# Optimization experiments

Measured on AMD Instinct MI355X. Metric: run time of the kernel, lower is better.

Reference implementation:

```python
import jax, jax.numpy as jnp
import numpy as np
from jax import lax

HEADS, DIM_HEAD = 4, 64
INNER = HEADS * DIM_HEAD              # 256
FEAT_DIM = MAP_DIM = OUT_DIM = 128
EXPANDED = 4 * OUT_DIM                # 512 (MBConv expansion)
MAP_SIZE = (8, 8, 8)
EPS = 1e-5


def conv3d(x, w, groups=1):
    # x: NCDHW, w: OIDHW ([out, in/groups, kd, kh, kw]); stride 1, 'same' padding
    return lax.conv_general_dilated(x, w, (1, 1, 1), 'SAME',
                                    feature_group_count=groups,
                                    dimension_numbers=('NCDHW', 'OIDHW', 'NCDHW'))


def inorm(x):
    # InstanceNorm3d (affine=False): normalize over spatial dims per sample/channel
    m = x.mean((2, 3, 4), keepdims=True)
    v = ((x - m) ** 2).mean((2, 3, 4), keepdims=True)
    return (x - m) * lax.rsqrt(v + EPS)


def _split_heads(t, spatial):
    # 'b (dim_head heads) d h w -> b heads (d h w) dim_head'
    B = t.shape[0]
    N = spatial[0] * spatial[1] * spatial[2]
    return t.reshape(B, DIM_HEAD, HEADS, N).transpose(0, 2, 3, 1)


def _merge_heads(t, spatial):
    # 'b heads n dim_head -> b (dim_head heads) d h w'
    B = t.shape[0]
    return t.transpose(0, 3, 1, 2).reshape(B, DIM_HEAD * HEADS, *spatial)


def setup_inputs() -> dict:
    key = jax.random.key(0)
    ks = jax.random.split(key, 16)
    r = lambda k, s: jax.random.normal(k, s, jnp.float32) * 0.05
    return {
        'x': jax.random.normal(ks[0], (2, FEAT_DIM, 24, 24, 24), jnp.float32),
        'semantic_map': jax.random.normal(ks[1], (2, MAP_DIM) + MAP_SIZE, jnp.float32),
        'w_fqv_dw': r(ks[2], (FEAT_DIM, 1, 3, 3, 3)),
        'w_fqv_pw': r(ks[3], (2 * INNER, FEAT_DIM, 1, 1, 1)),
        'w_mqv':    r(ks[4], (2 * INNER, MAP_DIM, 1, 1, 1)),
        'w_fout_dw': r(ks[5], (INNER, 1, 3, 3, 3)),
        'w_fout_pw': r(ks[6], (OUT_DIM, INNER, 1, 1, 1)),
        'w_mout':   r(ks[7], (MAP_DIM, INNER, 1, 1, 1)),
        'w_exp':    r(ks[8], (EXPANDED, OUT_DIM, 1, 1, 1)),
        'w_dw':     r(ks[9], (EXPANDED, 1, 3, 3, 3)),
        'w_se1':    r(ks[10], (EXPANDED // 4, EXPANDED, 1, 1, 1)),
        'b_se1':    jnp.zeros((EXPANDED // 4,), jnp.float32),
        'w_se2':    r(ks[11], (EXPANDED, EXPANDED // 4, 1, 1, 1)),
        'b_se2':    jnp.zeros((EXPANDED,), jnp.float32),
        'w_pw':     r(ks[12], (OUT_DIM, EXPANDED, 1, 1, 1)),
    }


def _mbconv(x, w_exp, w_dw, w_se1, b_se1, w_se2, b_se2, w_pw):
    # MBConv (preact ConvNormAct blocks, InstanceNorm + ReLU, SE, identity shortcut)
    h = conv3d(jax.nn.relu(inorm(x)), w_exp)
    h = conv3d(jax.nn.relu(inorm(h)), w_dw, groups=EXPANDED)
    s = h.mean((2, 3, 4), keepdims=True)                       # squeeze
    s = jax.nn.relu(conv3d(s, w_se1) + b_se1[None, :, None, None, None])
    s = jax.nn.sigmoid(conv3d(s, w_se2) + b_se2[None, :, None, None, None])
    h = h * s
    h = conv3d(inorm(h), w_pw)                                 # pointwise, act=False
    return h + x


def reference(x, semantic_map, w_fqv_dw, w_fqv_pw, w_mqv, w_fout_dw, w_fout_pw,
              w_mout, w_exp, w_dw, w_se1, b_se1, w_se2, b_se2, w_pw):
    B, C, D, H, W = x.shape
    feat = inorm(x)
    m = inorm(semantic_map)

    # QV projections: depthwise-separable for feat, 1x1 for map
    fqv = conv3d(conv3d(feat, w_fqv_dw, groups=FEAT_DIM), w_fqv_pw)
    fq, fv = jnp.split(fqv, 2, axis=1)
    mqv = conv3d(m, w_mqv)
    mq, mv = jnp.split(mqv, 2, axis=1)

    fq = _split_heads(fq, (D, H, W))   # [B, h, Nf, dh]
    fv = _split_heads(fv, (D, H, W))
    mq = _split_heads(mq, MAP_SIZE)    # [B, h, Nm, dh]
    mv = _split_heads(mv, MAP_SIZE)

    # shared score matrix, dual-direction softmax
    attn = jnp.einsum('bhid,bhjd->bhij', fq, mq) * (DIM_HEAD ** -0.5)
    feat_map_attn = jax.nn.softmax(attn, axis=-1)   # over map tokens j
    map_feat_attn = jax.nn.softmax(attn, axis=-2)   # over feat tokens i

    feat_out = jnp.einsum('bhij,bhjd->bhid', feat_map_attn, mv)   # [B,h,Nf,dh]
    map_out = jnp.einsum('bhji,bhjd->bhid', map_feat_attn, fv)    # [B,h,Nm,dh]

    feat_out = _merge_heads(feat_out, (D, H, W))
    map_out = _merge_heads(map_out, MAP_SIZE)

    feat_out = conv3d(conv3d(feat_out, w_fout_dw, groups=INNER), w_fout_pw)
    map_out = conv3d(map_out, w_mout)

    out = feat_out + x   # shortcut is identity (feat_dim == out_dim)
    out = _mbconv(out, w_exp, w_dw, w_se1, b_se1, w_se2, b_se2, w_pw)
    map_out = map_out + semantic_map
    return out, map_out
```

## Files before the change

### kernel.cpp

```cpp
#include <hip/hip_runtime.h>
#include <hip/hip_bf16.h>
#include <cstddef>

#define NF 13824
#define NM 512
#define NIC 27

typedef __attribute__((ext_vector_type(8))) short bf16x8;
typedef __attribute__((ext_vector_type(4))) float f32x4;

__device__ __forceinline__ void gload16(const float* g, float* l){
  __builtin_amdgcn_global_load_lds((const __attribute__((address_space(1))) void*)g,
                                   (__attribute__((address_space(3))) void*)l, 16, 0, 0);
}

__global__ void k_transpose6(const float* __restrict__ s0, float* __restrict__ d0,
                             const float* __restrict__ s1, float* __restrict__ d1,
                             const float* __restrict__ s2, float* __restrict__ d2,
                             const float* __restrict__ s3, float* __restrict__ d3,
                             const float* __restrict__ s4, float* __restrict__ d4,
                             const float* __restrict__ s5, float* __restrict__ d5){
  const float* W; float* WT; int Cout, Cin;
  switch (blockIdx.y){
    case 0: W=s0; WT=d0; Cout=512; Cin=128; break;
// ... 113 lines not shown

  {
    float4* l4 = (float4*)lds;
    float4 z = make_float4(0.f,0.f,0.f,0.f);
    for (int i=threadIdx.x; i<(4+26*728)/4; i+=256) l4[i] = z;
  }
  __syncthreads();

  const float* pin = in + (size_t)bc*NF;
  for (int i=threadIdx.x; i<NF/4; i+=256){
    int n = i*4;
    int d = n/576, r2 = n%576;
    int h = r2/24, wq = r2%24;
    float4 v = *(const float4*)(pin + n);
    float v0 = a*v.x+bb, v1 = a*v.y+bb, v2 = a*v.z+bb, v3 = a*v.w+bb;
    if (relu){ v0=fmaxf(v0,0.f); v1=fmaxf(v1,0.f); v2=fmaxf(v2,0.f); v3=fmaxf(v3,0.f); }
    *(float4*)(lds + 4 + (d+1)*728 + (h+1)*28 + wq) = make_float4(v0,v1,v2,v3);
  }

  const float* wc = w + c*27;
  float wr[27];
  #pragma unroll
  for (int k=0;k<27;k++) wr[k] = wc[k];
  __syncthreads();

  float ss=0.f, sq=0.f;
  for (int r = threadIdx.x; r < 576; r += 256){
    int d = r/24, h = r%24;
    float acc[24];
    #pragma unroll
    for (int i=0;i<24;i++) acc[i] = 0.f;
    #pragma unroll
    for (int kd=0;kd<3;kd++){
      #pragma unroll
      for (int kh=0;kh<3;kh++){
        const float* row = lds + 4 + (d+kd)*728 + (h+kh)*28;
        float rr[24];
        #pragma unroll
        for (int q=0;q<6;q++){
          float4 v4 = *(const float4*)(row + 4*q);
          rr[4*q]=v4.x; rr[4*q+1]=v4.y; rr[4*q+2]=v4.z; rr[4*q+3]=v4.w;
        }
        float rl = row[-1];
        float rrgt = row[24];
        float w0 = wr[kd*9+kh*3+0], w1 = wr[kd*9+kh*3+1], w2 = wr[kd*9+kh*3+2];
        acc[0] += w0*rl + w1*rr[0] + w2*rr[1];
        #pragma unroll
        for (int i=1;i<23;i++) acc[i] += w0*rr[i-1] + w1*rr[i] + w2*rr[i+1];
        acc[23] += w0*rr[22] + w1*rr[23] + w2*rrgt;
      }
    }
    if (stout){
      #pragma unroll
      for (int i=0;i<24;i++){ ss += acc[i]; sq += acc[i]*acc[i]; }
    }
    float* op = out + (size_t)bc*NF + r*24;
    #pragma unroll
    for (int q=0;q<6;q++)
      *(float4*)(op + 4*q) = make_float4(acc[4*q],acc[4*q+1],acc[4*q+2],acc[4*q+3]);
  }
  if (stout){
    rs2[threadIdx.x]=ss; rq2[threadIdx.x]=sq;
    __syncthreads();
    for (int o=128;o>0;o>>=1){
      if (threadIdx.x<o){ rs2[threadIdx.x]+=rs2[threadIdx.x+o]; rq2[threadIdx.x]+=rq2[threadIdx.x+o]; }
      __syncthreads();
    }
    if (threadIdx.x==0){
      float m = rs2[0]/NF;
      float v = rq2[0]/NF - m*m;
      stout[bc] = make_float2(m, v>0.f? v:0.f);
    }
  }
}

__global__ __launch_bounds__(256) void k_pw2(const float* __restrict__ in, const float* __restrict__ Wt,
                    const float* __restrict__ bias,
                    int Cin, int Cout, int N, int wstride,
                    const float* __restrict__ res,
                    float* __restrict__ out0,
                    __hip_bfloat16* __restrict__ qnm, __hip_bfloat16* __restrict__ vdm,
                    int mode, float2* __restrict__ part, int nparts){
  int b = blockIdx.z;
  int n0 = blockIdx.x*64, co0 = blockIdx.y*64;
  int tx = threadIdx.x & 15, ty = threadIdx.x >> 4;
  int wv = threadIdx.x >> 6, ln = threadIdx.x & 63;
  __shared__ float wl[2][2048];
  __shared__ float il[2][2048];
  float acc[4][4] = {};
  const float* inb = in + (size_t)b*Cin*N;
  const float* wb  = Wt + (size_t)b*wstride;

  int row0 = wv*8 + (ln>>4), col = (ln&15)*4;
  int row1 = row0 + 4;
  const float* gw0 = wb  + (size_t)row0*Cout + co0 + col;
  const float* gw1 = wb  + (size_t)row1*Cout + co0 + col;
  const float* gi0 = inb + (size_t)row0*N + n0 + col;
  const float* gi1 = inb + (size_t)row1*N + n0 + col;
  int lb0 = wv*512, lb1 = wv*512 + 256;

  gload16(gw0, &wl[0][lb0]); gload16(gw1, &wl[0][lb1]);
  gload16(gi0, &il[0][lb0]); gload16(gi1, &il[0][lb1]);
  __syncthreads();

  int nc = Cin >> 5;
  int cur = 0;
  for (int c=0; c<nc; c++){
    if (c+1 < nc){
      size_t ow = (size_t)(c+1)*32*Cout, oi = (size_t)(c+1)*32*N;
      gload16(gw0+ow, &wl[cur^1][lb0]); gload16(gw1+ow, &wl[cur^1][lb1]);
      gload16(gi0+oi, &il[cur^1][lb0]); gload16(gi1+oi, &il[cur^1][lb1]);
    }
    #pragma unroll
    for (int ci=0;ci<32;ci++){
      float4 a4 = *(const float4*)&wl[cur][ci*64 + ty*4];
      float4 b4 = *(const float4*)&il[cur][ci*64 + tx*4];
      acc[0][0]+=a4.x*b4.x; acc[0][1]+=a4.x*b4.y; acc[0][2]+=a4.x*b4.z; acc[0][3]+=a4.x*b4.w;
      acc[1][0]+=a4.y*b4.x; acc[1][1]+=a4.y*b4.y; acc[1][2]+=a4.y*b4.z; acc[1][3]+=a4.y*b4.w;
      acc[2][0]+=a4.z*b4.x; acc[2][1]+=a4.z*b4.y; acc[2][2]+=a4.z*b4.z; acc[2][3]+=a4.z*b4.w;
      acc[3][0]+=a4.w*b4.x; acc[3][1]+=a4.w*b4.y; acc[3][2]+=a4.w*b4.z; acc[3][3]+=a4.w*b4.w;
    }
    __syncthreads();
    cur ^= 1;
  }

  if (mode==0){
    #pragma unroll
    for (int i=0;i<4;i++){
      int co = co0 + ty*4 + i;
      float bco = bias ? bias[b*Cout + co] : 0.f;
      float* op = out0 + ((size_t)b*Cout + co)*N;
      float sv=0.f, qv=0.f;
      #pragma unroll
      for (int j=0;j<4;j++){
        int n = n0 + tx*4 + j;
        float v = acc[i][j] + bco;
        if (res) v += res[((size_t)b*Cout + co)*N + n];
        op[n] = v;
        sv += v; qv += v*v;
      }
      if (part){
        sv += __shfl_xor(sv,1); sv += __shfl_xor(sv,2); sv += __shfl_xor(sv,4); sv += __shfl_xor(sv,8);
        qv += __shfl_xor(qv,1); qv += __shfl_xor(qv,2); qv += __shfl_xor(qv,4); qv += __shfl_xor(qv,8);
        if (tx==0)
          part[(size_t)(b*Cout + co)*nparts + blockIdx.x] = make_float2(sv, qv);
      }
    }
  } else {
    int ccbase = (co0 & 255) + ty*4;
    int dd = ccbase >> 2;
    bool isq = (co0 < 256);
    #pragma unroll
    for (int i=0;i<4;i++){
      int bhid = b*4 + i;
      #pragma unroll
      for (int j=0;j<4;j++){
        int n = n0 + tx*4 + j;
        __hip_bfloat16 v = __float2bfloat16(acc[i][j]);
        if (isq) qnm[((size_t)bhid*N + n)*64 + dd] = v;
        else     vdm[((size_t)(bhid*64 + dd))*N + n] = v;
      }
    }
  }
}

__global__ __launch_bounds__(256) void k_pw(const float* __restrict__ in, const float* __restrict__ WT,
                    const float2* __restrict__ tf, int relu,
                    int Cin, int Cout, int N,
                    const float* __restrict__ res,
                    float* __restrict__ out0,
                    __hip_bfloat16* __restrict__ qnm, __hip_bfloat16* __restrict__ vdm,
                    int mode){
  int b = blockIdx.z;
  int n0 = blockIdx.x*64, co0 = blockIdx.y*64;
  int tx = threadIdx.x & 15, ty = threadIdx.x >> 4;
  int cc = threadIdx.x & 63, g = threadIdx.x >> 6;
  __shared__ float wl[32][68];
  __shared__ float il[32][68];
  float acc[4][4] = {};
  const float* inb = in + (size_t)b*Cin*N;

  float rw[8], rv[8], ta[8], tb[8];
  #pragma unroll
  for (int rr=0;rr<8;rr++){ ta[rr]=1.f; tb[rr]=0.f; }
  #pragma unroll
  for (int rr=0;rr<8;rr++){
    int ci = g + 4*rr;
    rw[rr] = WT[(size_t)ci*Cout + co0 + cc];
    rv[rr] = inb[(size_t)ci*N + n0 + cc];
    if (tf){ float2 t = tf[b*Cin + ci]; ta[rr]=t.x; tb[rr]=t.y; }
  }

  for (int c0=0;c0<Cin;c0+=32){
    __syncthreads();
    #pragma unroll
    for (int rr=0;rr<8;rr++){
      int ci = g + 4*rr;
      wl[ci][cc] = rw[rr];
      float v = ta[rr]*rv[rr] + tb[rr];
      if (relu) v = fmaxf(v, 0.f);
      il[ci][cc] = v;
    }
    __syncthreads();
    if (c0+32 < Cin){
      int c0n = c0+32;
      #pragma unroll
      for (int rr=0;rr<8;rr++){
        int ci = g + 4*rr;
        rw[rr] = WT[(size_t)(c0n+ci)*Cout + co0 + cc];
        rv[rr] = inb[(size_t)(c0n+ci)*N + n0 + cc];
        if (tf){ float2 t = tf[b*Cin + c0n + ci]; ta[rr]=t.x; tb[rr]=t.y; }
      }
    }
    #pragma unroll
    for (int ci=0;ci<32;ci++){
      float4 a4 = *(const float4*)&wl[ci][ty*4];
      float4 b4 = *(const float4*)&il[ci][tx*4];
      acc[0][0]+=a4.x*b4.x; acc[0][1]+=a4.x*b4.y; acc[0][2]+=a4.x*b4.z; acc[0][3]+=a4.x*b4.w;
      acc[1][0]+=a4.y*b4.x; acc[1][1]+=a4.y*b4.y; acc[1][2]+=a4.y*b4.z; acc[1][3]+=a4.y*b4.w;
      acc[2][0]+=a4.z*b4.x; acc[2][1]+=a4.z*b4.y; acc[2][2]+=a4.z*b4.z; acc[2][3]+=a4.z*b4.w;
      acc[3][0]+=a4.w*b4.x; acc[3][1]+=a4.w*b4.y; acc[3][2]+=a4.w*b4.z; acc[3][3]+=a4.w*b4.w;
    }
  }
  if (mode==0){
    #pragma unroll
    for (int i=0;i<4;i++){
      int co = co0 + ty*4 + i;
      float* op = out0 + ((size_t)b*Cout + co)*N;
      #pragma unroll
      for (int j=0;j<4;j++){
        int n = n0 + tx*4 + j;
        float v = acc[i][j];
        if (res) v += res[((size_t)b*Cout + co)*N + n];
        op[n] = v;
      }
    }
  } else {
    int ccbase = (co0 & 255) + ty*4;
    int dd = ccbase >> 2;
    bool isq = (co0 < 256);
    #pragma unroll
    for (int i=0;i<4;i++){
      int bhid = b*4 + i;
      #pragma unroll
      for (int j=0;j<4;j++){
        int n = n0 + tx*4 + j;
        __hip_bfloat16 v = __float2bfloat16(acc[i][j]);
        if (isq) qnm[((size_t)bhid*N + n)*64 + dd] = v;
        else     vdm[((size_t)(bhid*64 + dd))*N + n] = v;
      }
    }
  }
}

__global__ __launch_bounds__(256) void k_fattn(const __hip_bfloat16* __restrict__ qf,
    const __hip_bfloat16* __restrict__ qm, const __hip_bfloat16* __restrict__ vm,
    float* __restrict__ fo){
  int bh = blockIdx.y, b = bh>>2, h = bh&3;
  int w = threadIdx.x>>6, l = threadIdx.x&63;
  int i0 = blockIdx.x*128 + w*32;
  int lr = l&15, lg = l>>4;
  __shared__ __hip_bfloat16 pl[4][2][2][16][40];
  __shared__ float rsl[4][32];
  bf16x8 aq[2][2];
  #pragma unroll
  for (int g=0; g<2; g++){
    const __hip_bfloat16* qb = qf + ((size_t)bh*NF + i0 + g*16 + lr)*64 + lg*8;
    aq[g][0] = *(const bf16x8*)(qb);
    aq[g][1] = *(const bf16x8*)(qb + 32);
  }
  f32x4 facc[2][4];
  #pragma unroll
  for (int g=0; g<2; g++)
    #pragma unroll
    for (int t=0;t<4;t++){ facc[g][t][0]=0.f; facc[g][t][1]=0.f; facc[g][t][2]=0.f; facc[g][t][3]=0.f; }
  float rs[2][4] = {};
  const __hip_bfloat16* kbase = qm + ((size_t)bh*NM + lr)*64 + lg*8;
  const __hip_bfloat16* vbase = vm + ((size_t)bh*64 + lr)*NM + lg*8;

  auto fcomp = [&](bf16x8 K0, bf16x8 K1, bf16x8 K2, bf16x8 K3,
                   bf16x8 V0, bf16x8 V1, bf16x8 V2, bf16x8 V3, int SET){
    #pragma unroll
    for (int g=0; g<2; g++){
      f32x4 s0 = {0.f,0.f,0.f,0.f}, s1 = {0.f,0.f,0.f,0.f};
      s0 = __builtin_amdgcn_mfma_f32_16x16x32_bf16(aq[g][0], K0, s0, 0,0,0);
      s0 = __builtin_amdgcn_mfma_f32_16x16x32_bf16(aq[g][1], K1, s0, 0,0,0);
      s1 = __builtin_amdgcn_mfma_f32_16x16x32_bf16(aq[g][0], K2, s1, 0,0,0);
      s1 = __builtin_amdgcn_mfma_f32_16x16x32_bf16(aq[g][1], K3, s1, 0,0,0);
      #pragma unroll
      for (int r=0;r<4;r++){
        float p0 = __expf(s0[r]*0.125f);
        float p1 = __expf(s1[r]*0.125f);
        pl[w][SET][g][4*lg+r][lr]    = __float2bfloat16(p0);
        pl[w][SET][g][4*lg+r][16+lr] = __float2bfloat16(p1);
        rs[g][r] += p0 + p1;
      }
    }
    #pragma unroll
    for (int g=0; g<2; g++){
      bf16x8 bp = *(const bf16x8*)&pl[w][SET][g][lr][lg*8];
      facc[g][0] = __builtin_amdgcn_mfma_f32_16x16x32_bf16(V0, bp, facc[g][0], 0,0,0);
      facc[g][1] = __builtin_amdgcn_mfma_f32_16x16x32_bf16(V1, bp, facc[g][1], 0,0,0);
      facc[g][2] = __builtin_amdgcn_mfma_f32_16x16x32_bf16(V2, bp, facc[g][2], 0,0,0);
      facc[g][3] = __builtin_amdgcn_mfma_f32_16x16x32_bf16(V3, bp, facc[g][3], 0,0,0);
    }
  };

  bf16x8 kA0,kA1,kA2,kA3,vA0,vA1,vA2,vA3;
  bf16x8 kB0,kB1,kB2,kB3,vB0,vB1,vB2,vB3;
  #define FLOAD(KP,VP,J0) \
    KP##0 = *(const bf16x8*)(kbase + (size_t)(J0)*64); \
    KP##1 = *(const bf16x8*)(kbase + (size_t)(J0)*64 + 32); \
    KP##2 = *(const bf16x8*)(kbase + (size_t)(J0)*64 + 1024); \
    KP##3 = *(const bf16x8*)(kbase + (size_t)(J0)*64 + 1056); \
    VP##0 = *(const bf16x8*)(vbase + (J0)); \
    VP##1 = *(const bf16x8*)(vbase + 16*NM + (J0)); \
    VP##2 = *(const bf16x8*)(vbase + 32*NM + (J0)); \
    VP##3 = *(const bf16x8*)(vbase + 48*NM + (J0));

  FLOAD(kA,vA,0)
  for (int jt=0; jt<16; jt+=2){
    FLOAD(kB,vB,(jt+1)*32)
    fcomp(kA0,kA1,kA2,kA3,vA0,vA1,vA2,vA3,0);
    if (jt+2 < 16){ FLOAD(kA,vA,(jt+2)*32) }
    fcomp(kB0,kB1,kB2,kB3,vB0,vB1,vB2,vB3,1);
  }
  #undef FLOAD

  #pragma unroll
  for (int g=0; g<2; g++)
    #pragma unroll
    for (int r=0;r<4;r++){
      float v = rs[g][r];
      v += __shfl_xor(v,1); v += __shfl_xor(v,2); v += __shfl_xor(v,4); v += __shfl_xor(v,8);
      if (lr==0) rsl[w][g*16 + 4*lg+r] = v;
    }
  __syncthreads();
  #pragma unroll
  for (int g=0; g<2; g++){
    float inv = 1.f / rsl[w][g*16 + lr];
    #pragma unroll
    for (int dt=0; dt<4; dt++){
      #pragma unroll
      for (int r=0;r<4;r++){
        int d = dt*16 + 4*lg + r;
        fo[((size_t)(b*256 + d*4 + h))*NF + i0 + g*16 + lr] = facc[g][dt][r]*inv;
      }
    }
  }
}

__global__ __launch_bounds__(256) void k_mattn(const __hip_bfloat16* __restrict__ qm,
    const __hip_bfloat16* __restrict__ qf, const __hip_bfloat16* __restrict__ vf,
    float* __restrict__ num, float* __restrict__ cs){
  int ic = blockIdx.x, jb = blockIdx.y, bh = blockIdx.z;
  int w = threadIdx.x>>6, l = threadIdx.x&63;
  int lr = l&15, lg = l>>4;
  int jt0 = jb*128 + w*16;
  int jt1 = jt0 + 64;
  __shared__ __hip_bfloat16 pl[4][2][2][16][40];
  bf16x8 am[2][2];
  {
    const __hip_bfloat16* ab0 = qm + ((size_t)bh*NM + jt0 + lr)*64 + lg*8;
    const __hip_bfloat16* ab1 = qm + ((size_t)bh*NM + jt1 + lr)*64 + lg*8;
    am[0][0] = *(const bf16x8*)(ab0);
    am[0][1] = *(const bf16x8*)(ab0 + 32);
    am[1][0] = *(const bf16x8*)(ab1);
    am[1][1] = *(const bf16x8*)(ab1 + 32);
  }
  f32x4 macc[2][4];
  #pragma unroll
  for (int jg=0;jg<2;jg++)
    #pragma unroll
    for (int t=0;t<4;t++){ macc[jg][t][0]=0.f; macc[jg][t][1]=0.f; macc[jg][t][2]=0.f; macc[jg][t][3]=0.f; }
  float csr[2][4] = {};
  const __hip_bfloat16* fbase  = qf + ((size_t)bh*NF + lr)*64 + lg*8;
  const __hip_bfloat16* vfbase = vf + ((size_t)bh*64 + lr)*NF + lg*8;

  auto mcomp = [&](bf16x8 F0, bf16x8 F1, bf16x8 F2, bf16x8 F3,
                   bf16x8 V0, bf16x8 V1, bf16x8 V2, bf16x8 V3, int SET){
    #pragma unroll
    for (int jg=0;jg<2;jg++){
      f32x4 s0 = {0.f,0.f,0.f,0.f}, s1 = {0.f,0.f,0.f,0.f};
      s0 = __builtin_amdgcn_mfma_f32_16x16x32_bf16(am[jg][0], F0, s0, 0,0,0);
      s0 = __builtin_amdgcn_mfma_f32_16x16x32_bf16(am[jg][1], F1, s0, 0,0,0);
      s1 = __builtin_amdgcn_mfma_f32_16x16x32_bf16(am[jg][0], F2, s1, 0,0,0);
      s1 = __builtin_amdgcn_mfma_f32_16x16x32_bf16(am[jg][1], F3, s1, 0,0,0);
      #pragma unroll
      for (int r=0;r<4;r++){
        float p0 = __expf(s0[r]*0.125f);
        float p1 = __expf(s1[r]*0.125f);
        pl[w][SET][jg][4*lg+r][lr]    = __float2bfloat16(p0);
        pl[w][SET][jg][4*lg+r][16+lr] = __float2bfloat16(p1);
        csr[jg][r] += p0 + p1;
      }
    }
    #pragma unroll
    for (int jg=0;jg<2;jg++){
      bf16x8 bp = *(const bf16x8*)&pl[w][SET][jg][lr][lg*8];
      macc[jg][0] = __builtin_amdgcn_mfma_f32_16x16x32_bf16(V0, bp, macc[jg][0], 0,0,0);
      macc[jg][1] = __builtin_amdgcn_mfma_f32_16x16x32_bf16(V1, bp, macc[jg][1], 0,0,0);
      macc[jg][2] = __builtin_amdgcn_mfma_f32_16x16x32_bf16(V2, bp, macc[jg][2], 0,0,0);
      macc[jg][3] = __builtin_amdgcn_mfma_f32_16x16x32_bf16(V3, bp, macc[jg][3], 0,0,0);
    }
  };

  bf16x8 fA0,fA1,fA2,fA3,vA0,vA1,vA2,vA3;
  bf16x8 fB0,fB1,fB2,fB3,vB0,vB1,vB2,vB3;
  #define MLOAD(FP,VP,I0) \
    FP##0 = *(const bf16x8*)(fbase + (size_t)(I0)*64); \
    FP##1 = *(const bf16x8*)(fbase + (size_t)(I0)*64 + 32); \
    FP##2 = *(const bf16x8*)(fbase + (size_t)(I0)*64 + 1024); \
    FP##3 = *(const bf16x8*)(fbase + (size_t)(I0)*64 + 1056); \
    VP##0 = *(const bf16x8*)(vfbase + (size_t)(I0)); \
    VP##1 = *(const bf16x8*)(vfbase + (size_t)16*NF + (I0)); \
    VP##2 = *(const bf16x8*)(vfbase + (size_t)32*NF + (I0)); \
    VP##3 = *(const bf16x8*)(vfbase + (size_t)48*NF + (I0));

  int ibase = ic*512;
  MLOAD(fA,vA, ibase)
  for (int is=0; is<16; is+=2){
    MLOAD(fB,vB, ibase + (is+1)*32)
    mcomp(fA0,fA1,fA2,fA3,vA0,vA1,vA2,vA3,0);
    if (is+2<16){ MLOAD(fA,vA, ibase + (is+2)*32) }
    mcomp(fB0,fB1,fB2,fB3,vB0,vB1,vB2,vB3,1);
  }
  #undef MLOAD

  size_t nb = ((size_t)(ic*8 + bh)*64)*512;
  #pragma unroll
  for (int jg=0;jg<2;jg++){
    int jt = jg ? jt1 : jt0;
    #pragma unroll
    for (int dt=0;dt<4;dt++){
      #pragma unroll
      for (int r=0;r<4;r++){
        num[nb + (size_t)(dt*16 + 4*lg + r)*512 + jt + lr] = macc[jg][dt][r];
      }
    }
  }
  #pragma unroll
  for (int jg=0;jg<2;jg++){
    int jt = jg ? jt1 : jt0;
    #pragma unroll
    for (int r=0;r<4;r++){
      float v = csr[jg][r];
      v += __shfl_xor(v,1); v += __shfl_xor(v,2); v += __shfl_xor(v,4); v += __shfl_xor(v,8);
      if (lr==0) cs[(size_t)(ic*8 + bh)*512 + jt + 4*lg + r] = v;
    }
  }
}

__global__ void k_comb(const float* __restrict__ num, const float* __restrict__ cs,
                       float* __restrict__ ma){
  int idx = blockIdx.x*256 + threadIdx.x;
  if (idx >= 8*512*64) return;
  int bh = idx>>15; int rem = idx&32767; int j = rem>>6; int d = rem&63;
  float s=0.f, c=0.f;
  for (int ic=0;ic<NIC;ic++){
    s += num[((size_t)(ic*8+bh)*64 + d)*512 + j];
    c += cs[(size_t)(ic*8+bh)*512 + j];
  }
  int b = bh>>2, h = bh&3;
  ma[((size_t)(b*256 + d*4 + h))*NM + j] = s/c;
}

__global__ void k_se(const float2* __restrict__ st, const float* __restrict__ w1, const float* __restrict__ b1,
                     const float* __restrict__ w2, const float* __restrict__ b2, float* __restrict__ sout){
  int b = blockIdx.x; int t = threadIdx.x;
  __shared__ float mean[512]; __shared__ float s1[128];
  mean[t]     = st[b*512 + t].x;
  mean[t+256] = st[b*512 + t + 256].x;
  __syncthreads();
  if (t<128){
    float a = b1[t];
    for (int c=0;c<512;c++) a += w1[t*512+c]*mean[c];
    s1[t] = fmaxf(a, 0.f);
  }
  __syncthreads();
  for (int o=t;o<512;o+=256){
    float a = b2[o];
    for (int c=0;c<128;c++) a += w2[o*128+c]*s1[c];
    sout[b*512+o] = 1.f/(1.f+__expf(-a));
  }
}

extern "C" void kernel_launch(void* const* d_in, const int* in_sizes, int n_in,
                              void* d_out, int out_size, void* d_ws, size_t ws_size,
                              hipStream_t stream){
  const float* x     = (const float*)d_in[0];
  const float* smap  = (const float*)d_in[1];
  const float* wfdw  = (const float*)d_in[2];
  const float* wfpw  = (const float*)d_in[3];
  const float* wmqv  = (const float*)d_in[4];
  const float* wodw  = (const float*)d_in[5];
  const float* wopw  = (const float*)d_in[6];
  const float* wmout = (const float*)d_in[7];
  const float* wexp  = (const float*)d_in[8];
  const float* wdw   = (const float*)d_in[9];
  const float* wse1  = (const float*)d_in[10];
  const float* bse1  = (const float*)d_in[11];
  const float* wse2  = (const float*)d_in[12];
  const float* bse2  = (const float*)d_in[13];
  const float* wpw   = (const float*)d_in[14];

  float* out  = (float*)d_out;
  float* mout = out + (size_t)2*128*NF;

  float* W = (float*)d_ws;
  size_t o = 0;
  __hip_bfloat16* qf = (__hip_bfloat16*)(W + o); o += (size_t)8*NF*32;
  __hip_bfloat16* vf = (__hip_bfloat16*)(W + o); o += (size_t)8*NF*32;
  float* fdw  = W + o; o += (size_t)2*128*NF;
  float* num  = W + o; o += (size_t)NIC*8*64*512;
  __hip_bfloat16* qm = (__hip_bfloat16*)(W + o); o += 8*NM*32;
  __hip_bfloat16* vm = (__hip_bfloat16*)(W + o); o += 8*NM*32;
  float* csb  = W + o; o += (size_t)NIC*8*512;
  float* ma   = W + o; o += (size_t)2*256*NM;
  float* h2   = (float*)d_ws;
  float* fo   = W + o; o += (size_t)2*256*NF;
  float* fdw2 = W + o; o += (size_t)2*256*NF;
  float* h1 = fo;
  float* wTf  = W + o; o += 512*128;
  float* wTm  = W + o; o += 512*128;
  float* wTo  = W + o; o += 128*256;
  float* wTmo = W + o; o += 128*256;
  float* wTe  = W + o; o += 512*128;
  float* wTp  = W + o; o += 128*512;
  float* wfP  = W + o; o += (size_t)2*512*128;
  float* biasP= W + o; o += 2*128;
  float2* partO = (float2*)(W+o); o += (size_t)2*256*216;
  float2* partH1= (float2*)(W+o); o += (size_t)2*1024*216;
  float2* tfO = (float2*)(W+o); o += 512;
  float2* tfH1= (float2*)(W+o); o += 2048;
  float2* stA = (float2*)(W+o); o += 512;
  float2* tfA = (float2*)(W+o); o += 512;
  float2* stM = (float2*)(W+o); o += 512;
  float2* tfM = (float2*)(W+o); o += 512;
  float2* stH2= (float2*)(W+o); o += 2048;
  float2* tfH = (float2*)(W+o); o += 2048;
  float* sbuf = W + o; o += 1024;
  (void)ws_size; (void)in_sizes; (void)n_in; (void)out_size;

  k_transpose6<<<dim3(256,6),256,0,stream>>>(wfpw,wTf, wmqv,wTm, wopw,wTo, wmout,wTmo, wexp,wTe, wpw,wTp);

  k_stats<<<256,256,0,stream>>>(x, stA, NF, tfA);
  k_dw3t<<<256,256,0,stream>>>(x, wfdw, tfA, fdw, 128, 0, nullptr);
  k_pw2<<<dim3(216,8,2),256,0,stream>>>(fdw, wTf, nullptr, 128,512,NF,0, nullptr, nullptr, qf, vf, 1, nullptr,0);

  k_stats<<<256,256,0,stream>>>(smap, stM, NM, tfM);
  k_pw<<<dim3(8,8,2),256,0,stream>>>(smap, wTm, tfM,0, 128,512,NM, nullptr, nullptr, qm, vm, 1);

  k_fattn<<<dim3(108,8),256,0,stream>>>(qf, qm, vm, fo);
  k_mattn<<<dim3(NIC,4,8),256,0,stream>>>(qm, qf, vf, num, csb);
  k_comb<<<1024,256,0,stream>>>(num, csb, ma);

  k_dw3t<<<512,256,0,stream>>>(fo, wodw, nullptr, fdw2, 256, 0, nullptr);
  k_pw2<<<dim3(216,2,2),256,0,stream>>>(fdw2, wTo, nullptr, 256,128,NF,0, x, out, nullptr,nullptr, 0, partO,216);
  k_pw<<<dim3(8,2,2),256,0,stream>>>(ma, wTmo, nullptr,0, 256,128,NM, smap, mout, nullptr,nullptr, 0);

  k_red<<<64,256,0,stream>>>(partO, 216, 256, 1.f/NF, tfO);
  k_act<<<3456,256,0,stream>>>(out, tfO, fdw);
  k_pw2<<<dim3(216,8,2),256,0,stream>>>(fdw, wTe, nullptr, 128,512,NF,0, nullptr, h1, nullptr,nullptr, 0, partH1,216);

  k_red<<<256,256,0,stream>>>(partH1, 216, 1024, 1.f/NF, tfH1);
  k_dw3t<<<1024,256,0,stream>>>(h1, wdw, tfH1, h2, 512, 1, stH2);

  k_se<<<2,256,0,stream>>>(stH2, wse1,bse1,wse2,bse2, sbuf);
  k_make_tf<<<4,256,0,stream>>>(stH2, sbuf, tfH, 1024);
  k_fold<<<dim3(128,2),256,0,stream>>>(wTp, tfH, wfP, biasP);
  k_pw2<<<dim3(216,2,2),256,0,stream>>>(h2, wfP, biasP, 512,128,NF,512*128, out, out, nullptr,nullptr, 0, nullptr,0);
}
```

Before: 575.8 us.

## Widen pointwise GEMM tiles to 128 channels and fuse both attention kernels

The pointwise conv kernel now computes 128 output channels per block with an 8x4 per-thread accumulator tile. Each loaded activation tile is reused across twice as many channels, halving the grid and the redundant input reads. The feature-to-map and map-to-feature attention kernels are merged into one launch with interleaved block roles, which removes a launch and lets the two workloads overlap. The costs are higher register pressure and fewer blocks for the pointwise GEMMs, and the fused kernel takes on the larger register footprint of the two branches.

```diff
diff --git a/kernel.cpp b/kernel.cpp
--- a/kernel.cpp
+++ b/kernel.cpp
@@ -219,43 +219,53 @@
                     __hip_bfloat16* __restrict__ qnm, __hip_bfloat16* __restrict__ vdm,
                     int mode, float2* __restrict__ part, int nparts){
   int b = blockIdx.z;
-  int n0 = blockIdx.x*64, co0 = blockIdx.y*64;
-  int tx = threadIdx.x & 15, ty = threadIdx.x >> 4;
-  int wv = threadIdx.x >> 6, ln = threadIdx.x & 63;
-  __shared__ float wl[2][2048];
-  __shared__ float il[2][2048];
-  float acc[4][4] = {};
+  int n0 = blockIdx.x*64, co0 = blockIdx.y*128;
+  int t = threadIdx.x;
+  int tx = t & 15, tyy = t >> 4;
+  int wv = t >> 6, ln = t & 63;
+  __shared__ float wl[2][32*128];
+  __shared__ float il[2][32*64];
+  float acc[8][4] = {};
   const float* inb = in + (size_t)b*Cin*N;
   const float* wb  = Wt + (size_t)b*wstride;
 
-  int row0 = wv*8 + (ln>>4), col = (ln&15)*4;
-  int row1 = row0 + 4;
-  const float* gw0 = wb  + (size_t)row0*Cout + co0 + col;
-  const float* gw1 = wb  + (size_t)row1*Cout + co0 + col;
-  const float* gi0 = inb + (size_t)row0*N + n0 + col;
-  const float* gi1 = inb + (size_t)row1*N + n0 + col;
-  int lb0 = wv*512, lb1 = wv*512 + 256;
-
-  gload16(gw0, &wl[0][lb0]); gload16(gw1, &wl[0][lb1]);
-  gload16(gi0, &il[0][lb0]); gload16(gi1, &il[0][lb1]);
+  int wrow = (ln>>5), wcol = (ln&31)*4;
+  int irow = (ln>>4), icol = (ln&15)*4;
+
+  auto STAGE = [&](int c0, int buf){
+    #pragma unroll
+    for (int k=0;k<4;k++){
+      int row = wv*8 + 2*k + wrow;
+      gload16(wb + (size_t)(c0+row)*Cout + co0 + wcol, &wl[buf][row*128 + wcol]);
+    }
+    #pragma unroll
+    for (int k=0;k<2;k++){
+      int row = wv*8 + 4*k + irow;
+      gload16(inb + (size_t)(c0+row)*N + n0 + icol, &il[buf][row*64 + icol]);
+    }
+  };
+
+  STAGE(0, 0);
   __syncthreads();
 
   int nc = Cin >> 5;
   int cur = 0;
   for (int c=0; c<nc; c++){
-    if (c+1 < nc){
-      size_t ow = (size_t)(c+1)*32*Cout, oi = (size_t)(c+1)*32*N;
-      gload16(gw0+ow, &wl[cur^1][lb0]); gload16(gw1+ow, &wl[cur^1][lb1]);
-      gload16(gi0+oi, &il[cur^1][lb0]); gload16(gi1+oi, &il[cur^1][lb1]);
-    }
+    if (c+1 < nc) STAGE((c+1)*32, cur^1);
     #pragma unroll
     for (int ci=0;ci<32;ci++){
-      float4 a4 = *(const float4*)&wl[cur][ci*64 + ty*4];
+      const float* wr2 = &wl[cur][ci*128 + tyy*8];
+      float4 w0 = *(const float4*)(wr2);
+      float4 w1 = *(const float4*)(wr2+4);
       float4 b4 = *(const float4*)&il[cur][ci*64 + tx*4];
-      acc[0][0]+=a4.x*b4.x; acc[0][1]+=a4.x*b4.y; acc[0][2]+=a4.x*b4.z; acc[0][3]+=a4.x*b4.w;
-      acc[1][0]+=a4.y*b4.x; acc[1][1]+=a4.y*b4.y; acc[1][2]+=a4.y*b4.z; acc[1][3]+=a4.y*b4.w;
-      acc[2][0]+=a4.z*b4.x; acc[2][1]+=a4.z*b4.y; acc[2][2]+=a4.z*b4.z; acc[2][3]+=a4.z*b4.w;
-      acc[3][0]+=a4.w*b4.x; acc[3][1]+=a4.w*b4.y; acc[3][2]+=a4.w*b4.z; acc[3][3]+=a4.w*b4.w;
+      acc[0][0]+=w0.x*b4.x; acc[0][1]+=w0.x*b4.y; acc[0][2]+=w0.x*b4.z; acc[0][3]+=w0.x*b4.w;
+      acc[1][0]+=w0.y*b4.x; acc[1][1]+=w0.y*b4.y; acc[1][2]+=w0.y*b4.z; acc[1][3]+=w0.y*b4.w;
+      acc[2][0]+=w0.z*b4.x; acc[2][1]+=w0.z*b4.y; acc[2][2]+=w0.z*b4.z; acc[2][3]+=w0.z*b4.w;
+      acc[3][0]+=w0.w*b4.x; acc[3][1]+=w0.w*b4.y; acc[3][2]+=w0.w*b4.z; acc[3][3]+=w0.w*b4.w;
+      acc[4][0]+=w1.x*b4.x; acc[4][1]+=w1.x*b4.y; acc[4][2]+=w1.x*b4.z; acc[4][3]+=w1.x*b4.w;
+      acc[5][0]+=w1.y*b4.x; acc[5][1]+=w1.y*b4.y; acc[5][2]+=w1.y*b4.z; acc[5][3]+=w1.y*b4.w;
+      acc[6][0]+=w1.z*b4.x; acc[6][1]+=w1.z*b4.y; acc[6][2]+=w1.z*b4.z; acc[6][3]+=w1.z*b4.w;
+      acc[7][0]+=w1.w*b4.x; acc[7][1]+=w1.w*b4.y; acc[7][2]+=w1.w*b4.z; acc[7][3]+=w1.w*b4.w;
     }
     __syncthreads();
     cur ^= 1;
@@ -263,8 +273,8 @@
 
   if (mode==0){
     #pragma unroll
-    for (int i=0;i<4;i++){
-      int co = co0 + ty*4 + i;
+    for (int i=0;i<8;i++){
+      int co = co0 + tyy*8 + i;
       float bco = bias ? bias[b*Cout + co] : 0.f;
       float* op = out0 + ((size_t)b*Cout + co)*N;
       float sv=0.f, qv=0.f;
@@ -284,12 +294,12 @@
       }
     }
   } else {
-    int ccbase = (co0 & 255) + ty*4;
-    int dd = ccbase >> 2;
     bool isq = (co0 < 256);
     #pragma unroll
-    for (int i=0;i<4;i++){
-      int bhid = b*4 + i;
+    for (int i=0;i<8;i++){
+      int co = co0 + tyy*8 + i;
+      int head = co & 3, dd = (co & 255) >> 2;
+      int bhid = b*4 + head;
       #pragma unroll
       for (int j=0;j<4;j++){
         int n = n0 + tx*4 + j;
@@ -390,200 +400,199 @@
   }
 }
 
-__global__ __launch_bounds__(256) void k_fattn(const __hip_bfloat16* __restrict__ qf,
+__global__ __launch_bounds__(256) void k_attn(const __hip_bfloat16* __restrict__ qf,
     const __hip_bfloat16* __restrict__ qm, const __hip_bfloat16* __restrict__ vm,
-    float* __restrict__ fo){
-  int bh = blockIdx.y, b = bh>>2, h = bh&3;
-  int w = threadIdx.x>>6, l = threadIdx.x&63;
-  int i0 = blockIdx.x*128 + w*32;
-  int lr = l&15, lg = l>>4;
+    const __hip_bfloat16* __restrict__ vf,
+    float* __restrict__ fo, float* __restrict__ num, float* __restrict__ cs){
   __shared__ __hip_bfloat16 pl[4][2][2][16][40];
   __shared__ float rsl[4][32];
-  bf16x8 aq[2][2];
-  #pragma unroll
-  for (int g=0; g<2; g++){
-    const __hip_bfloat16* qb = qf + ((size_t)bh*NF + i0 + g*16 + lr)*64 + lg*8;
-    aq[g][0] = *(const bf16x8*)(qb);
-    aq[g][1] = *(const bf16x8*)(qb + 32);
-  }
-  f32x4 facc[2][4];
-  #pragma unroll
-  for (int g=0; g<2; g++)
-    #pragma unroll
-    for (int t=0;t<4;t++){ facc[g][t][0]=0.f; facc[g][t][1]=0.f; facc[g][t][2]=0.f; facc[g][t][3]=0.f; }
-  float rs[2][4] = {};
-  const __hip_bfloat16* kbase = qm + ((size_t)bh*NM + lr)*64 + lg*8;
-  const __hip_bfloat16* vbase = vm + ((size_t)bh*64 + lr)*NM + lg*8;
-
-  auto fcomp = [&](bf16x8 K0, bf16x8 K1, bf16x8 K2, bf16x8 K3,
-                   bf16x8 V0, bf16x8 V1, bf16x8 V2, bf16x8 V3, int SET){
-    #pragma unroll
-    for (int g=0; g<2; g++){
-      f32x4 s0 = {0.f,0.f,0.f,0.f}, s1 = {0.f,0.f,0.f,0.f};
-      s0 = __builtin_amdgcn_mfma_f32_16x16x32_bf16(aq[g][0], K0, s0, 0,0,0);
-      s0 = __builtin_amdgcn_mfma_f32_16x16x32_bf16(aq[g][1], K1, s0, 0,0,0);
-      s1 = __builtin_amdgcn_mfma_f32_16x16x32_bf16(aq[g][0], K2, s1, 0,0,0);
-      s1 = __builtin_amdgcn_mfma_f32_16x16x32_bf16(aq[g][1], K3, s1, 0,0,0);
-      #pragma unroll
-      for (int r=0;r<4;r++){
-        float p0 = __expf(s0[r]*0.125f);
-        float p1 = __expf(s1[r]*0.125f);
-        pl[w][SET][g][4*lg+r][lr]    = __float2bfloat16(p0);
-        pl[w][SET][g][4*lg+r][16+lr] = __float2bfloat16(p1);
-        rs[g][r] += p0 + p1;
-      }
-    }
-    #pragma unroll
-    for (int g=0; g<2; g++){
-      bf16x8 bp = *(const bf16x8*)&pl[w][SET][g][lr][lg*8];
-      facc[g][0] = __builtin_amdgcn_mfma_f32_16x16x32_bf16(V0, bp, facc[g][0], 0,0,0);
-      facc[g][1] = __builtin_amdgcn_mfma_f32_16x16x32_bf16(V1, bp, facc[g][1], 0,0,0);
-      facc[g][2] = __builtin_amdgcn_mfma_f32_16x16x32_bf16(V2, bp, facc[g][2], 0,0,0);
-      facc[g][3] = __builtin_amdgcn_mfma_f32_16x16x32_bf16(V3, bp, facc[g][3], 0,0,0);
-    }
-  };
-
-  bf16x8 kA0,kA1,kA2,kA3,vA0,vA1,vA2,vA3;
-  bf16x8 kB0,kB1,kB2,kB3,vB0,vB1,vB2,vB3;
-  #define FLOAD(KP,VP,J0) \
-    KP##0 = *(const bf16x8*)(kbase + (size_t)(J0)*64); \
-    KP##1 = *(const bf16x8*)(kbase + (size_t)(J0)*64 + 32); \
-    KP##2 = *(const bf16x8*)(kbase + (size_t)(J0)*64 + 1024); \
-    KP##3 = *(const bf16x8*)(kbase + (size_t)(J0)*64 + 1056); \
-    VP##0 = *(const bf16x8*)(vbase + (J0)); \
-    VP##1 = *(const bf16x8*)(vbase + 16*NM + (J0)); \
-    VP##2 = *(const bf16x8*)(vbase + 32*NM + (J0)); \
-    VP##3 = *(const bf16x8*)(vbase + 48*NM + (J0));
-
-  FLOAD(kA,vA,0)
-  for (int jt=0; jt<16; jt+=2){
-    FLOAD(kB,vB,(jt+1)*32)
-    fcomp(kA0,kA1,kA2,kA3,vA0,vA1,vA2,vA3,0);
-    if (jt+2 < 16){ FLOAD(kA,vA,(jt+2)*32) }
-    fcomp(kB0,kB1,kB2,kB3,vB0,vB1,vB2,vB3,1);
-  }
-  #undef FLOAD
-
-  #pragma unroll
-  for (int g=0; g<2; g++)
-    #pragma unroll
-    for (int r=0;r<4;r++){
-      float v = rs[g][r];
-      v += __shfl_xor(v,1); v += __shfl_xor(v,2); v += __shfl_xor(v,4); v += __shfl_xor(v,8);
-      if (lr==0) rsl[w][g*16 + 4*lg+r] = v;
-    }
-  __syncthreads();
-  #pragma unroll
-  for (int g=0; g<2; g++){
-    float inv = 1.f / rsl[w][g*16 + lr];
-    #pragma unroll
-    for (int dt=0; dt<4; dt++){
-      #pragma unroll
-      for (int r=0;r<4;r++){
-        int d = dt*16 + 4*lg + r;
-        fo[((size_t)(b*256 + d*4 + h))*NF + i0 + g*16 + lr] = facc[g][dt][r]*inv;
-      }
-    }
-  }
-}
-
-__global__ __launch_bounds__(256) void k_mattn(const __hip_bfloat16* __restrict__ qm,
-    const __hip_bfloat16* __restrict__ qf, const __hip_bfloat16* __restrict__ vf,
-    float* __restrict__ num, float* __restrict__ cs){
-  int ic = blockIdx.x, jb = blockIdx.y, bh = blockIdx.z;
+  int bid = blockIdx.x;
+  int sub = bid >> 1;
   int w = threadIdx.x>>6, l = threadIdx.x&63;
   int lr = l&15, lg = l>>4;
-  int jt0 = jb*128 + w*16;
-  int jt1 = jt0 + 64;
-  __shared__ __hip_bfloat16 pl[4][2][2][16][40];
-  bf16x8 am[2][2];
-  {
-    const __hip_bfloat16* ab0 = qm + ((size_t)bh*NM + jt0 + lr)*64 + lg*8;
-    const __hip_bfloat16* ab1 = qm + ((size_t)bh*NM + jt1 + lr)*64 + lg*8;
-    am[0][0] = *(const bf16x8*)(ab0);
-    am[0][1] = *(const bf16x8*)(ab0 + 32);
-    am[1][0] = *(const bf16x8*)(ab1);
-    am[1][1] = *(const bf16x8*)(ab1 + 32);
-  }
-  f32x4 macc[2][4];
-  #pragma unroll
-  for (int jg=0;jg<2;jg++)
-    #pragma unroll
-    for (int t=0;t<4;t++){ macc[jg][t][0]=0.f; macc[jg][t][1]=0.f; macc[jg][t][2]=0.f; macc[jg][t][3]=0.f; }
-  float csr[2][4] = {};
-  const __hip_bfloat16* fbase  = qf + ((size_t)bh*NF + lr)*64 + lg*8;
-  const __hip_bfloat16* vfbase = vf + ((size_t)bh*64 + lr)*NF + lg*8;
-
-  auto mcomp = [&](bf16x8 F0, bf16x8 F1, bf16x8 F2, bf16x8 F3,
-                   bf16x8 V0, bf16x8 V1, bf16x8 V2, bf16x8 V3, int SET){
+
+  if (bid & 1){
+    int bh = sub/108, b = bh>>2, h = bh&3;
+    int i0 = (sub%108)*128 + w*32;
+    bf16x8 aq[2][2];
+    #pragma unroll
+    for (int g=0; g<2; g++){
+      const __hip_bfloat16* qb = qf + ((size_t)bh*NF + i0 + g*16 + lr)*64 + lg*8;
+      aq[g][0] = *(const bf16x8*)(qb);
+      aq[g][1] = *(const bf16x8*)(qb + 32);
+    }
+    f32x4 facc[2][4];
+    #pragma unroll
+    for (int g=0; g<2; g++)
+      #pragma unroll
+      for (int t=0;t<4;t++){ facc[g][t][0]=0.f; facc[g][t][1]=0.f; facc[g][t][2]=0.f; facc[g][t][3]=0.f; }
+    float rs[2][4] = {};
+    const __hip_bfloat16* kbase = qm + ((size_t)bh*NM + lr)*64 + lg*8;
+    const __hip_bfloat16* vbase = vm + ((size_t)bh*64 + lr)*NM + lg*8;
+
+    auto fcomp = [&](bf16x8 K0, bf16x8 K1, bf16x8 K2, bf16x8 K3,
+                     bf16x8 V0, bf16x8 V1, bf16x8 V2, bf16x8 V3, int SET){
+      #pragma unroll
+      for (int g=0; g<2; g++){
+        f32x4 s0 = {0.f,0.f,0.f,0.f}, s1 = {0.f,0.f,0.f,0.f};
+        s0 = __builtin_amdgcn_mfma_f32_16x16x32_bf16(aq[g][0], K0, s0, 0,0,0);
+        s0 = __builtin_amdgcn_mfma_f32_16x16x32_bf16(aq[g][1], K1, s0, 0,0,0);
+        s1 = __builtin_amdgcn_mfma_f32_16x16x32_bf16(aq[g][0], K2, s1, 0,0,0);
+        s1 = __builtin_amdgcn_mfma_f32_16x16x32_bf16(aq[g][1], K3, s1, 0,0,0);
+        #pragma unroll
+        for (int r=0;r<4;r++){
+          float p0 = __expf(s0[r]*0.125f);
+          float p1 = __expf(s1[r]*0.125f);
+          pl[w][SET][g][4*lg+r][lr]    = __float2bfloat16(p0);
+          pl[w][SET][g][4*lg+r][16+lr] = __float2bfloat16(p1);
+          rs[g][r] += p0 + p1;
+        }
+      }
+      #pragma unroll
+      for (int g=0; g<2; g++){
+        bf16x8 bp = *(const bf16x8*)&pl[w][SET][g][lr][lg*8];
+        facc[g][0] = __builtin_amdgcn_mfma_f32_16x16x32_bf16(V0, bp, facc[g][0], 0,0,0);
+        facc[g][1] = __builtin_amdgcn_mfma_f32_16x16x32_bf16(V1, bp, facc[g][1], 0,0,0);
+        facc[g][2] = __builtin_amdgcn_mfma_f32_16x16x32_bf16(V2, bp, facc[g][2], 0,0,0);
+        facc[g][3] = __builtin_amdgcn_mfma_f32_16x16x32_bf16(V3, bp, facc[g][3], 0,0,0);
+      }
+    };
+
+    bf16x8 kA0,kA1,kA2,kA3,vA0,vA1,vA2,vA3;
+    bf16x8 kB0,kB1,kB2,kB3,vB0,vB1,vB2,vB3;
+    #define FLOAD(KP,VP,J0) \
+      KP##0 = *(const bf16x8*)(kbase + (size_t)(J0)*64); \
+      KP##1 = *(const bf16x8*)(kbase + (size_t)(J0)*64 + 32); \
+      KP##2 = *(const bf16x8*)(kbase + (size_t)(J0)*64 + 1024); \
+      KP##3 = *(const bf16x8*)(kbase + (size_t)(J0)*64 + 1056); \
+      VP##0 = *(const bf16x8*)(vbase + (J0)); \
+      VP##1 = *(const bf16x8*)(vbase + 16*NM + (J0)); \
+      VP##2 = *(const bf16x8*)(vbase + 32*NM + (J0)); \
+      VP##3 = *(const bf16x8*)(vbase + 48*NM + (J0));
+
+    FLOAD(kA,vA,0)
+    for (int jt=0; jt<16; jt+=2){
+      FLOAD(kB,vB,(jt+1)*32)
+      fcomp(kA0,kA1,kA2,kA3,vA0,vA1,vA2,vA3,0);
+      if (jt+2 < 16){ FLOAD(kA,vA,(jt+2)*32) }
+      fcomp(kB0,kB1,kB2,kB3,vB0,vB1,vB2,vB3,1);
+    }
+    #undef FLOAD
+
+    #pragma unroll
+    for (int g=0; g<2; g++)
+      #pragma unroll
+      for (int r=0;r<4;r++){
+        float v = rs[g][r];
+        v += __shfl_xor(v,1); v += __shfl_xor(v,2); v += __shfl_xor(v,4); v += __shfl_xor(v,8);
+        if (lr==0) rsl[w][g*16 + 4*lg+r] = v;
+      }
+    __syncthreads();
+    #pragma unroll
+    for (int g=0; g<2; g++){
+      float inv = 1.f / rsl[w][g*16 + lr];
+      #pragma unroll
+      for (int dt=0; dt<4; dt++){
+        #pragma unroll
+        for (int r=0;r<4;r++){
+          int d = dt*16 + 4*lg + r;
+          fo[((size_t)(b*256 + d*4 + h))*NF + i0 + g*16 + lr] = facc[g][dt][r]*inv;
+        }
+      }
+    }
+  } else {
+    int ic = sub%27, jb = (sub/27)&3, bh = sub/108;
+    int jt0 = jb*128 + w*16;
+    int jt1 = jt0 + 64;
+    bf16x8 am[2][2];
+    {
+      const __hip_bfloat16* ab0 = qm + ((size_t)bh*NM + jt0 + lr)*64 + lg*8;
+      const __hip_bfloat16* ab1 = qm + ((size_t)bh*NM + jt1 + lr)*64 + lg*8;
+      am[0][0] = *(const bf16x8*)(ab0);
+      am[0][1] = *(const bf16x8*)(ab0 + 32);
+      am[1][0] = *(const bf16x8*)(ab1);
+      am[1][1] = *(const bf16x8*)(ab1 + 32);
+    }
+    f32x4 macc[2][4];
+    #pragma unroll
+    for (int jg=0;jg<2;jg++)
+      #pragma unroll
+      for (int t=0;t<4;t++){ macc[jg][t][0]=0.f; macc[jg][t][1]=0.f; macc[jg][t][2]=0.f; macc[jg][t][3]=0.f; }
+    float csr[2][4] = {};
+    const __hip_bfloat16* fbase  = qf + ((size_t)bh*NF + lr)*64 + lg*8;
+    const __hip_bfloat16* vfbase = vf + ((size_t)bh*64 + lr)*NF + lg*8;
+
+    auto mcomp = [&](bf16x8 F0, bf16x8 F1, bf16x8 F2, bf16x8 F3,
+                     bf16x8 V0, bf16x8 V1, bf16x8 V2, bf16x8 V3, int SET){
+      #pragma unroll
+      for (int jg=0;jg<2;jg++){
+        f32x4 s0 = {0.f,0.f,0.f,0.f}, s1 = {0.f,0.f,0.f,0.f};
+        s0 = __builtin_amdgcn_mfma_f32_16x16x32_bf16(am[jg][0], F0, s0, 0,0,0);
+        s0 = __builtin_amdgcn_mfma_f32_16x16x32_bf16(am[jg][1], F1, s0, 0,0,0);
+        s1 = __builtin_amdgcn_mfma_f32_16x16x32_bf16(am[jg][0], F2, s1, 0,0,0);
+        s1 = __builtin_amdgcn_mfma_f32_16x16x32_bf16(am[jg][1], F3, s1, 0,0,0);
+        #pragma unroll
+        for (int r=0;r<4;r++){
+          float p0 = __expf(s0[r]*0.125f);
+          float p1 = __expf(s1[r]*0.125f);
+          pl[w][SET][jg][4*lg+r][lr]    = __float2bfloat16(p0);
+          pl[w][SET][jg][4*lg+r][16+lr] = __float2bfloat16(p1);
+          csr[jg][r] += p0 + p1;
+        }
+      }
+      #pragma unroll
+      for (int jg=0;jg<2;jg++){
+        bf16x8 bp = *(const bf16x8*)&pl[w][SET][jg][lr][lg*8];
+        macc[jg][0] = __builtin_amdgcn_mfma_f32_16x16x32_bf16(V0, bp, macc[jg][0], 0,0,0);
+        macc[jg][1] = __builtin_amdgcn_mfma_f32_16x16x32_bf16(V1, bp, macc[jg][1], 0,0,0);
+        macc[jg][2] = __builtin_amdgcn_mfma_f32_16x16x32_bf16(V2, bp, macc[jg][2], 0,0,0);
+        macc[jg][3] = __builtin_amdgcn_mfma_f32_16x16x32_bf16(V3, bp, macc[jg][3], 0,0,0);
+      }
+    };
+
+    bf16x8 fA0,fA1,fA2,fA3,vA0,vA1,vA2,vA3;
+    bf16x8 fB0,fB1,fB2,fB3,vB0,vB1,vB2,vB3;
+    #define MLOAD(FP,VP,I0) \
+      FP##0 = *(const bf16x8*)(fbase + (size_t)(I0)*64); \
+      FP##1 = *(const bf16x8*)(fbase + (size_t)(I0)*64 + 32); \
+      FP##2 = *(const bf16x8*)(fbase + (size_t)(I0)*64 + 1024); \
+      FP##3 = *(const bf16x8*)(fbase + (size_t)(I0)*64 + 1056); \
+      VP##0 = *(const bf16x8*)(vfbase + (size_t)(I0)); \
+      VP##1 = *(const bf16x8*)(vfbase + (size_t)16*NF + (I0)); \
+      VP##2 = *(const bf16x8*)(vfbase + (size_t)32*NF + (I0)); \
+      VP##3 = *(const bf16x8*)(vfbase + (size_t)48*NF + (I0));
+
+    int ibase = ic*512;
+    MLOAD(fA,vA, ibase)
+    for (int is=0; is<16; is+=2){
+      MLOAD(fB,vB, ibase + (is+1)*32)
+      mcomp(fA0,fA1,fA2,fA3,vA0,vA1,vA2,vA3,0);
+      if (is+2<16){ MLOAD(fA,vA, ibase + (is+2)*32) }
+      mcomp(fB0,fB1,fB2,fB3,vB0,vB1,vB2,vB3,1);
+    }
+    #undef MLOAD
+
+    size_t nb = ((size_t)(ic*8 + bh)*64)*512;
     #pragma unroll
     for (int jg=0;jg<2;jg++){
-      f32x4 s0 = {0.f,0.f,0.f,0.f}, s1 = {0.f,0.f,0.f,0.f};
-      s0 = __builtin_amdgcn_mfma_f32_16x16x32_bf16(am[jg][0], F0, s0, 0,0,0);
-      s0 = __builtin_amdgcn_mfma_f32_16x16x32_bf16(am[jg][1], F1, s0, 0,0,0);
-      s1 = __builtin_amdgcn_mfma_f32_16x16x32_bf16(am[jg][0], F2, s1, 0,0,0);
-      s1 = __builtin_amdgcn_mfma_f32_16x16x32_bf16(am[jg][1], F3, s1, 0,0,0);
+      int jt = jg ? jt1 : jt0;
+      #pragma unroll
+      for (int dt=0;dt<4;dt++){
+        #pragma unroll
+        for (int r=0;r<4;r++){
+          num[nb + (size_t)(dt*16 + 4*lg + r)*512 + jt + lr] = macc[jg][dt][r];
+        }
+      }
+    }
+    #pragma unroll
+    for (int jg=0;jg<2;jg++){
+      int jt = jg ? jt1 : jt0;
       #pragma unroll
       for (int r=0;r<4;r++){
-        float p0 = __expf(s0[r]*0.125f);
-        float p1 = __expf(s1[r]*0.125f);
-        pl[w][SET][jg][4*lg+r][lr]    = __float2bfloat16(p0);
-        pl[w][SET][jg][4*lg+r][16+lr] = __float2bfloat16(p1);
-        csr[jg][r] += p0 + p1;
-      }
-    }
-    #pragma unroll
-    for (int jg=0;jg<2;jg++){
-      bf16x8 bp = *(const bf16x8*)&pl[w][SET][jg][lr][lg*8];
-      macc[jg][0] = __builtin_amdgcn_mfma_f32_16x16x32_bf16(V0, bp, macc[jg][0], 0,0,0);
-      macc[jg][1] = __builtin_amdgcn_mfma_f32_16x16x32_bf16(V1, bp, macc[jg][1], 0,0,0);
-      macc[jg][2] = __builtin_amdgcn_mfma_f32_16x16x32_bf16(V2, bp, macc[jg][2], 0,0,0);
-      macc[jg][3] = __builtin_amdgcn_mfma_f32_16x16x32_bf16(V3, bp, macc[jg][3], 0,0,0);
-    }
-  };
-
-  bf16x8 fA0,fA1,fA2,fA3,vA0,vA1,vA2,vA3;
-  bf16x8 fB0,fB1,fB2,fB3,vB0,vB1,vB2,vB3;
-  #define MLOAD(FP,VP,I0) \
-    FP##0 = *(const bf16x8*)(fbase + (size_t)(I0)*64); \
-    FP##1 = *(const bf16x8*)(fbase + (size_t)(I0)*64 + 32); \
-    FP##2 = *(const bf16x8*)(fbase + (size_t)(I0)*64 + 1024); \
-    FP##3 = *(const bf16x8*)(fbase + (size_t)(I0)*64 + 1056); \
-    VP##0 = *(const bf16x8*)(vfbase + (size_t)(I0)); \
-    VP##1 = *(const bf16x8*)(vfbase + (size_t)16*NF + (I0)); \
-    VP##2 = *(const bf16x8*)(vfbase + (size_t)32*NF + (I0)); \
-    VP##3 = *(const bf16x8*)(vfbase + (size_t)48*NF + (I0));
-
-  int ibase = ic*512;
-  MLOAD(fA,vA, ibase)
-  for (int is=0; is<16; is+=2){
-    MLOAD(fB,vB, ibase + (is+1)*32)
-    mcomp(fA0,fA1,fA2,fA3,vA0,vA1,vA2,vA3,0);
-    if (is+2<16){ MLOAD(fA,vA, ibase + (is+2)*32) }
-    mcomp(fB0,fB1,fB2,fB3,vB0,vB1,vB2,vB3,1);
-  }
-  #undef MLOAD
-
-  size_t nb = ((size_t)(ic*8 + bh)*64)*512;
-  #pragma unroll
-  for (int jg=0;jg<2;jg++){
-    int jt = jg ? jt1 : jt0;
-    #pragma unroll
-    for (int dt=0;dt<4;dt++){
-      #pragma unroll
-      for (int r=0;r<4;r++){
-        num[nb + (size_t)(dt*16 + 4*lg + r)*512 + jt + lr] = macc[jg][dt][r];
-      }
-    }
-  }
-  #pragma unroll
-  for (int jg=0;jg<2;jg++){
-    int jt = jg ? jt1 : jt0;
-    #pragma unroll
-    for (int r=0;r<4;r++){
-      float v = csr[jg][r];
-      v += __shfl_xor(v,1); v += __shfl_xor(v,2); v += __shfl_xor(v,4); v += __shfl_xor(v,8);
-      if (lr==0) cs[(size_t)(ic*8 + bh)*512 + jt + 4*lg + r] = v;
+        float v = csr[jg][r];
+        v += __shfl_xor(v,1); v += __shfl_xor(v,2); v += __shfl_xor(v,4); v += __shfl_xor(v,8);
+        if (lr==0) cs[(size_t)(ic*8 + bh)*512 + jt + 4*lg + r] = v;
+      }
     }
   }
 }
@@ -683,22 +692,21 @@
 
   k_stats<<<256,256,0,stream>>>(x, stA, NF, tfA);
   k_dw3t<<<256,256,0,stream>>>(x, wfdw, tfA, fdw, 128, 0, nullptr);
-  k_pw2<<<dim3(216,8,2),256,0,stream>>>(fdw, wTf, nullptr, 128,512,NF,0, nullptr, nullptr, qf, vf, 1, nullptr,0);
+  k_pw2<<<dim3(216,4,2),256,0,stream>>>(fdw, wTf, nullptr, 128,512,NF,0, nullptr, nullptr, qf, vf, 1, nullptr,0);
 
   k_stats<<<256,256,0,stream>>>(smap, stM, NM, tfM);
   k_pw<<<dim3(8,8,2),256,0,stream>>>(smap, wTm, tfM,0, 128,512,NM, nullptr, nullptr, qm, vm, 1);
 
-  k_fattn<<<dim3(108,8),256,0,stream>>>(qf, qm, vm, fo);
-  k_mattn<<<dim3(NIC,4,8),256,0,stream>>>(qm, qf, vf, num, csb);
+  k_attn<<<dim3(1728),256,0,stream>>>(qf, qm, vm, vf, fo, num, csb);
   k_comb<<<1024,256,0,stream>>>(num, csb, ma);
 
   k_dw3t<<<512,256,0,stream>>>(fo, wodw, nullptr, fdw2, 256, 0, nullptr);
-  k_pw2<<<dim3(216,2,2),256,0,stream>>>(fdw2, wTo, nullptr, 256,128,NF,0, x, out, nullptr,nullptr, 0, partO,216);
+  k_pw2<<<dim3(216,1,2),256,0,stream>>>(fdw2, wTo, nullptr, 256,128,NF,0, x, out, nullptr,nullptr, 0, partO,216);
   k_pw<<<dim3(8,2,2),256,0,stream>>>(ma, wTmo, nullptr,0, 256,128,NM, smap, mout, nullptr,nullptr, 0);
 
   k_red<<<64,256,0,stream>>>(partO, 216, 256, 1.f/NF, tfO);
   k_act<<<3456,256,0,stream>>>(out, tfO, fdw);
-  k_pw2<<<dim3(216,8,2),256,0,stream>>>(fdw, wTe, nullptr, 128,512,NF,0, nullptr, h1, nullptr,nullptr, 0, partH1,216);
+  k_pw2<<<dim3(216,4,2),256,0,stream>>>(fdw, wTe, nullptr, 128,512,NF,0, nullptr, h1, nullptr,nullptr, 0, partH1,216);
 
   k_red<<<256,256,0,stream>>>(partH1, 216, 1024, 1.f/NF, tfH1);
   k_dw3t<<<1024,256,0,stream>>>(h1, wdw, tfH1, h2, 512, 1, stH2);
@@ -706,5 +714,5 @@
   k_se<<<2,256,0,stream>>>(stH2, wse1,bse1,wse2,bse2, sbuf);
   k_make_tf<<<4,256,0,stream>>>(stH2, sbuf, tfH, 1024);
   k_fold<<<dim3(128,2),256,0,stream>>>(wTp, tfH, wfP, biasP);
-  k_pw2<<<dim3(216,2,2),256,0,stream>>>(h2, wfP, biasP, 512,128,NF,512*128, out, out, nullptr,nullptr, 0, nullptr,0);
-}
+  k_pw2<<<dim3(216,1,2),256,0,stream>>>(h2, wfP, biasP, 512,128,NF,512*128, out, out, nullptr,nullptr, 0, nullptr,0);
+}
```

Result: no change. 570.4 us (-0.9%).
